# Optimization experiments

Measured on AMD Instinct MI355X. Metric: run time of the kernel, lower is better.

Reference implementation:

```python
import jax, jax.numpy as jnp
import numpy as np

B, NP, FEAT, DEG, H = 16, 1024, 512, 16, 1024
E = B * NP * DEG
RATIO = 0.8


def setup_inputs() -> dict:
    key = jax.random.key(0)
    ks = jax.random.split(key, 16)
    x = jax.random.normal(ks[0], (B * NP, FEAT), jnp.float32)
    g = jnp.repeat(jnp.arange(B, dtype=jnp.int32), NP * DEG)
    src = jax.random.randint(ks[1], (E,), 0, NP, jnp.int32) + g * NP
    dst = jax.random.randint(ks[2], (E,), 0, NP, jnp.int32) + g * NP
    edge_index = jnp.stack([src, dst])
    batch = jnp.repeat(jnp.arange(B, dtype=jnp.int32), NP)
    sc = 0.02
    inp = dict(x=x, edge_index=edge_index, batch=batch)
    # SAGEConv params: out = lin_l(mean_agg) + lin_r(x); bias only on lin_l (PyG default)
    inp['W1l'] = sc * jax.random.normal(ks[3], (H, FEAT), jnp.float32)
    inp['b1'] = jnp.zeros((H,), jnp.float32)
    inp['W1r'] = sc * jax.random.normal(ks[4], (H, FEAT), jnp.float32)
    inp['p1'] = jax.random.normal(ks[5], (H,), jnp.float32)
    inp['W2l'] = sc * jax.random.normal(ks[6], (H, H), jnp.float32)
    inp['b2'] = jnp.zeros((H,), jnp.float32)
    inp['W2r'] = sc * jax.random.normal(ks[7], (H, H), jnp.float32)
    inp['p2'] = jax.random.normal(ks[8], (H,), jnp.float32)
    inp['W3l'] = sc * jax.random.normal(ks[9], (H, H), jnp.float32)
    inp['b3'] = jnp.zeros((H,), jnp.float32)
    inp['W3r'] = sc * jax.random.normal(ks[10], (H, H), jnp.float32)
    inp['p3'] = jax.random.normal(ks[11], (H,), jnp.float32)
    return inp


def _sage(x, src, dst, w, Wl, b, Wr, n_nodes):
    # mean aggregation over (masked) incoming edges, isolated nodes -> 0
    deg = jax.ops.segment_sum(w, dst, num_segments=n_nodes)
    agg = jax.ops.segment_sum(x[src] * w[:, None], dst, num_segments=n_nodes)
    mean = agg / jnp.maximum(deg, 1.0)[:, None]
    return mean @ Wl.T + b + x @ Wr.T


def _topk_pool(x, src, dst, mask, p, n_per):
    # PyG TopKPooling: score = tanh((x.w)/||w||); keep top ceil(ratio*n) per graph
    k = int(np.ceil(RATIO * n_per))
    s = jnp.tanh((x @ p) / jnp.linalg.norm(p))
    vals, idx = jax.lax.top_k(s.reshape(B, n_per), k)          # [B,k]
    old = (idx + (jnp.arange(B, dtype=idx.dtype) * n_per)[:, None]).reshape(-1)
    x_new = x[old] * vals.reshape(-1)[:, None]                  # gate kept nodes by score
    remap = jnp.full((B * n_per,), -1, jnp.int32).at[old].set(jnp.arange(B * k, dtype=jnp.int32))
    s2, d2 = remap[src], remap[dst]
    m2 = mask & (s2 >= 0) & (d2 >= 0)                           # drop edges losing an endpoint
    return x_new, jnp.where(m2, s2, 0), jnp.where(m2, d2, 0), m2, k


def _readout(x, n_per):
    xr = x.reshape(B, n_per, H)
    return jnp.concatenate([xr.max(axis=1), xr.mean(axis=1)], axis=1)  # [B, 2H]


def reference(x, edge_index, batch, W1l, b1, W1r, p1, W2l, b2, W2r, p2, W3l, b3, W3r, p3):
    src, dst = edge_index[0], edge_index[1]
    mask = jnp.ones((src.shape[0],), bool)
    n = NP
    h = jax.nn.relu(_sage(x, src, dst, mask.astype(x.dtype), W1l, b1, W1r, B * n))
    h, src, dst, mask, n = _topk_pool(h, src, dst, mask, p1, n)
    x1 = _readout(h, n)
    h = jax.nn.relu(_sage(h, src, dst, mask.astype(h.dtype), W2l, b2, W2r, B * n))
    h, src, dst, mask, n = _topk_pool(h, src, dst, mask, p2, n)
    x2 = _readout(h, n)
    h = jax.nn.relu(_sage(h, src, dst, mask.astype(h.dtype), W3l, b3, W3r, B * n))
    h, src, dst, mask, n = _topk_pool(h, src, dst, mask, p3, n)
    x3 = _readout(h, n)
    return x1 + x2 + x3
```

## Files before the change

### kernel.cpp

```cpp
#include <hip/hip_runtime.h>
#include <math.h>

#define B_    16
#define NP_   1024
#define FEAT_ 512
#define H_    1024
#define E_    262144
#define EPG_  16384
#define K1_   820
#define K2_   656
#define K3_   525
#define M1_   16384
#define M2_   13120
#define M3_   10496
#define MP1_  16384
#define MP2_  13312
#define MP3_  11264
#define SPROWS_ 16384

typedef unsigned short ushort_t;
typedef __bf16 bf16x8 __attribute__((ext_vector_type(8)));
typedef float f32x4 __attribute__((ext_vector_type(4)));

__device__ inline ushort_t f2bf(float f) {
    unsigned u = __float_as_uint(f);
    u += 0x7FFF + ((u >> 16) & 1);
    return (ushort_t)(u >> 16);
}
__device__ inline float bf2f(ushort_t h) {
    return __uint_as_float(((unsigned)h) << 16);
}
__device__ inline void split1(float v, ushort_t& hi, ushort_t& lo) {
    hi = f2bf(v);
    lo = f2bf(v - bf2f(hi));
}

__device__ inline void gll16(const void* g, void* l) {
    __builtin_amdgcn_global_load_lds((__attribute__((address_space(1))) void*)g,
                                     (__attribute__((address_space(3))) void*)l, 16, 0, 0);
}


__global__ __launch_bounds__(1024) void prep2_kernel(const int* __restrict__ ei,
                                                     int* __restrict__ counts,
                                                     int* __restrict__ offsets,
                                                     int* __restrict__ adj,
                                                     const float* __restrict__ p1,
                                                     const float* __restrict__ p2,
                                                     const float* __restrict__ p3,
                                                     float* __restrict__ pnout,
                                                     const float* __restrict__ W1l, const float* __restrict__ W1r,
                                                     const float* __restrict__ W2l, const float* __restrict__ W2r,
                                                     const float* __restrict__ W3l, const float* __restrict__ W3r,
                                                     ushort_t* __restrict__ Wb1, ushort_t* __restrict__ Wb2,
                                                     ushort_t* __restrict__ Wb3) {
    int t = threadIdx.x;
    if (blockIdx.x < 16) {
        __shared__ int cnt[1024];
        __shared__ int scanb[1024];
        int b = blockIdx.x;
        int e0 = b * EPG_;
        cnt[t] = 0;
        __syncthreads();
        for (int e = e0 + t; e < e0 + EPG_; e += 1024)
            atomicAdd(&cnt[ei[E_ + e] - b * NP_], 1);
        __syncthreads();
        int v = cnt[t];
        scanb[t] = v;
        __syncthreads();
        for (int off = 1; off < 1024; off <<= 1) {
            int tv = (t >= off) ? scanb[t - off] : 0;
            __syncthreads();
            scanb[t] += tv;
            __syncthreads();
        }
        int excl = scanb[t] - v;
        counts[b * NP_ + t] = v;
        offsets[b * NP_ + t] = e0 + excl;
        cnt[t] = excl;
        __syncthreads();
        for (int e = e0 + t; e < e0 + EPG_; e += 1024) {
            int s = ei[e];
            int dloc = ei[E_ + e] - b * NP_;
            int pos = atomicAdd(&cnt[dloc], 1);
            adj[e0 + pos] = s;
        }
        return;
    }
    if (blockIdx.x < 19) {
        const float* p = blockIdx.x == 16 ? p1 : (blockIdx.x == 17 ? p2 : p3);
        __shared__ float red[1024];
        float a = p[t];
        red[t] = a * a;
        __syncthreads();
        for (int s = 512; s > 0; s >>= 1) {
            if (t < s) red[t] += red[t + s];
            __syncthreads();
        }
        if (t == 0) pnout[blockIdx.x - 16] = sqrtf(red[0]);
        return;
    }
    int idx = (blockIdx.x - 19) * 1024 + t;
    if (idx >= 524288 + 1048576 + 1048576) return;
    const float *Wl, *Wr; ushort_t* Wbig; int K;
    if (idx < 524288) { Wl = W1l; Wr = W1r; Wbig = Wb1; K = 512; }
    else if (idx < 524288 + 1048576) { idx -= 524288; Wl = W2l; Wr = W2r; Wbig = Wb2; K = 1024; }
    else { idx -= 524288 + 1048576; Wl = W3l; Wr = W3r; Wbig = Wb3; K = 1024; }
    int n = idx / K;
    int k = idx - n * K;
    ushort_t* row = Wbig + (size_t)n * (4 * K);
    float a = Wl[idx];
    ushort_t ah = f2bf(a);
    row[k] = ah;
    row[K + k] = f2bf(a - bf2f(ah));
    float b = Wr[idx];
    ushort_t bh = f2bf(b);
    row[2 * K + k] = bh;
    row[3 * K + k] = f2bf(b - bf2f(bh));
}


__global__ __launch_bounds__(128) void agg1_k512(const float* __restrict__ x,
                                                 const int* __restrict__ adj,
                                                 const int* __restrict__ offsets,
                                                 const int* __restrict__ counts,
                                                 ushort_t* __restrict__ Abig) {
    int gid = blockIdx.x;
    int xcd = gid & 7;
    int u = gid >> 3;
    int half = u & 1;
    int pi = u >> 1;
    int gsel = (pi >= 512) ? 1 : 0;
    int g = xcd + (gsel << 3);
    int node = g * 1024 + (pi - (gsel << 9)) * 2 + (threadIdx.x >> 6);
    int c = threadIdx.x & 63;
    int col4 = half * 64 + c;
    int start = offsets[node], cnt = counts[node];
    float d = fmaxf((float)cnt, 1.0f);
    const float4* xb = (const float4*)x;
    float ax = 0.f, ay = 0.f, az = 0.f, aw = 0.f;
    int j = 0;
    for (; j + 8 <= cnt; j += 8) {
        int si[8];
#pragma unroll
        for (int q = 0; q < 8; ++q) si[q] = adj[start + j + q];
        float4 vv[8];
#pragma unroll
        for (int q = 0; q < 8; ++q) vv[q] = xb[(size_t)si[q] * 128 + col4];
#pragma unroll
        for (int q = 0; q < 8; ++q) {
            ax += vv[q].x; ay += vv[q].y; az += vv[q].z; aw += vv[q].w;
        }
    }
    for (; j + 4 <= cnt; j += 4) {
        int s0 = adj[start + j + 0], s1 = adj[start + j + 1];
        int s2 = adj[start + j + 2], s3 = adj[start + j + 3];
        float4 v0 = xb[(size_t)s0 * 128 + col4];
        float4 v1 = xb[(size_t)s1 * 128 + col4];
        float4 v2 = xb[(size_t)s2 * 128 + col4];
        float4 v3 = xb[(size_t)s3 * 128 + col4];
        ax += (v0.x + v1.x) + (v2.x + v3.x);
        ay += (v0.y + v1.y) + (v2.y + v3.y);
        az += (v0.z + v1.z) + (v2.z + v3.z);
        aw += (v0.w + v1.w) + (v2.w + v3.w);
    }
    for (; j < cnt; ++j) {
        float4 v = xb[(size_t)adj[start + j] * 128 + col4];
        ax += v.x; ay += v.y; az += v.z; aw += v.w;
    }
    float inv = 1.0f / d;
    float4 cv = xb[(size_t)node * 128 + col4];
    ushort_t* row = Abig + (size_t)node * 2048;
    int f = col4 * 4;
    ushort4 mh, ml, ch, cl;
    split1(ax * inv, mh.x, ml.x); split1(ay * inv, mh.y, ml.y);
    split1(az * inv, mh.z, ml.z); split1(aw * inv, mh.w, ml.w);
    split1(cv.x, ch.x, cl.x); split1(cv.y, ch.y, cl.y);
    split1(cv.z, ch.z, cl.z); split1(cv.w, ch.w, cl.w);
    *(ushort4*)&row[f]        = mh;
    *(ushort4*)&row[512 + f]  = ml;
    *(ushort4*)&row[1024 + f] = ch;
    *(ushort4*)&row[1536 + f] = cl;
}

template<int LAYER>
__global__ __launch_bounds__(128) void agg23_k1024(const float* __restrict__ h,
                                                   const int* __restrict__ adj,
                                                   const int* __restrict__ offsets,
                                                   const int* __restrict__ counts,
                                                   const int* __restrict__ old_idx,
                                                   const float* __restrict__ vals,
                                                   ushort_t* __restrict__ Abig,
                                                   int n_per, int M, int npad) {
    int gid = blockIdx.x;
    if (gid >= 32 * n_per) {
        int r = gid - 32 * n_per;
        if (r < npad) {
            uint4* row = (uint4*)(Abig + (size_t)(M + r) * 4096);
#pragma unroll
            for (int q = 0; q < 4; ++q) row[threadIdx.x + q * 128] = (uint4){0, 0, 0, 0};
        }
        return;
    }
    int xcd = gid & 7;
    int u = gid >> 3;
    int half = u & 1;
    int nl = u >> 1;
    int gsel = (nl >= n_per) ? 1 : 0;
    int g = xcd + (gsel << 3);
    int node = g * n_per + nl - gsel * n_per;
    int c = threadIdx.x;
    int col4 = half * 128 + c;
    int start = offsets[node], cnt = counts[node];
    float d = fmaxf((float)cnt, 1.0f);
    const float4* hb = (const float4*)h;
    float ax = 0.f, ay = 0.f, az = 0.f, aw = 0.f;
    int j = 0;
    for (; j + 8 <= cnt; j += 8) {
        int si[8];
#pragma unroll
        for (int q = 0; q < 8; ++q) si[q] = adj[start + j + q];
        int oi[8]; float wi[8];
#pragma unroll
        for (int q = 0; q < 8; ++q) { oi[q] = old_idx[si[q]]; wi[q] = vals[si[q]]; }
        float4 vv[8];
#pragma unroll
        for (int q = 0; q < 8; ++q) vv[q] = hb[(size_t)oi[q] * 256 + col4];
#pragma unroll
        for (int q = 0; q < 8; ++q) {
            ax += wi[q] * vv[q].x; ay += wi[q] * vv[q].y;
            az += wi[q] * vv[q].z; aw += wi[q] * vv[q].w;
        }
    }
    for (; j + 4 <= cnt; j += 4) {
        int s0 = adj[start + j + 0], s1 = adj[start + j + 1];
        int s2 = adj[start + j + 2], s3 = adj[start + j + 3];
        int o0 = old_idx[s0], o1 = old_idx[s1], o2 = old_idx[s2], o3 = old_idx[s3];
        float w0 = vals[s0], w1 = vals[s1], w2 = vals[s2], w3 = vals[s3];
        float4 v0 = hb[(size_t)o0 * 256 + col4];
        float4 v1 = hb[(size_t)o1 * 256 + col4];
        float4 v2 = hb[(size_t)o2 * 256 + col4];
        float4 v3 = hb[(size_t)o3 * 256 + col4];
        ax += (w0 * v0.x + w1 * v1.x) + (w2 * v2.x + w3 * v3.x);
        ay += (w0 * v0.y + w1 * v1.y) + (w2 * v2.y + w3 * v3.y);
        az += (w0 * v0.z + w1 * v1.z) + (w2 * v2.z + w3 * v3.z);
        aw += (w0 * v0.w + w1 * v1.w) + (w2 * v2.w + w3 * v3.w);
    }
    for (; j < cnt; ++j) {
        int s = adj[start + j];
        int o = old_idx[s];
        float w = vals[s];
        float4 v = hb[(size_t)o * 256 + col4];
        ax += w * v.x; ay += w * v.y; az += w * v.z; aw += w * v.w;
    }
    float inv = 1.0f / d;
    int on = old_idx[node];
    float vn = vals[node];
    float4 cv = hb[(size_t)on * 256 + col4];
    cv.x *= vn; cv.y *= vn; cv.z *= vn; cv.w *= vn;
    ushort_t* row = Abig + (size_t)node * 4096;
    int f = col4 * 4;
    ushort4 mh, ml, ch, cl;
    split1(ax * inv, mh.x, ml.x); split1(ay * inv, mh.y, ml.y);
    split1(az * inv, mh.z, ml.z); split1(aw * inv, mh.w, ml.w);
    split1(cv.x, ch.x, cl.x); split1(cv.y, ch.y, cl.y);
    split1(cv.z, ch.z, cl.z); split1(cv.w, ch.w, cl.w);
    *(ushort4*)&row[f]        = mh;
    *(ushort4*)&row[1024 + f] = ml;
    *(ushort4*)&row[2048 + f] = ch;
    *(ushort4*)&row[3072 + f] = cl;
}


#define STR_(x) #x
#define VMW2_(n) asm volatile("s_waitcnt vmcnt(" STR_(n) ")" ::: "memory")
#define VMW(n) VMW2_(n)
#define BARM() do { __builtin_amdgcn_s_barrier(); asm volatile("" ::: "memory"); } while (0)

#define STG(Lw_, pl_, src_, c_) {                                                   \
    const ushort_t* s_ = (src_) + (c_);                                             \
    gll16(s_, (Lw_) + (pl_) * 8192);                                                \
    gll16(s_ + rstep, (Lw_) + (pl_) * 8192 + 4096);                                 \
}

#define MFQ(I0, Aarr, A0, Barr)                                                     \
    _Pragma("unroll")                                                               \
    for (int ii = 0; ii < 4; ++ii) {                                                \
        _Pragma("unroll")                                                           \
        for (int jj = 0; jj < 4; ++jj)                                              \
            acc[(I0) + ii][jj] = __builtin_amdgcn_mfma_f32_16x16x32_bf16(           \
                Aarr[(A0) + ii], Barr[jj], acc[(I0) + ii][jj], 0, 0, 0);            \
    }

#define CHUNK(t_, b_, stg_, vb_, v1_, v3_) do {                                     \
    int cn_ = ((t_) + 1 < NC2) ? ((t_) + 1) * 32 : 2 * KK + ((t_) + 1 - NC2) * 32;  \
    const ushort_t* Lr = L + (b_) * 32768;                                          \
    ushort_t* Lw = L + (1 - (b_)) * 32768 + tid * 8;                                \
    VMW(vb_);                                                                       \
    BARM();                                                                         \
    bf16x8 ah[8], al[8], bh[4], bl[4];                                              \
    _Pragma("unroll") for (int q = 0; q < 4; ++q)                                   \
        ah[q] = *(const bf16x8*)&Lr[aoff + q * 512];                                \
    _Pragma("unroll") for (int q = 0; q < 4; ++q)                                   \
        bh[q] = *(const bf16x8*)&Lr[16384 + boff + q * 512];                        \
                           \
    _Pragma("unroll") for (int q = 0; q < 4; ++q)                                   \
        ah[4 + q] = *(const bf16x8*)&Lr[aoff + (4 + q) * 512];                      \
    if (stg_) { STG(Lw, 0, Ag, cn_); }                                              \
    BARM();                                                                         \
    __builtin_amdgcn_s_setprio(1);                                                  \
    MFQ(0, ah, 0, bh);                                                              \
    __builtin_amdgcn_s_setprio(0);                                                  \
    VMW(v1_);                                                                       \
    BARM();                                                                         \
                           \
    _Pragma("unroll") for (int q = 0; q < 4; ++q)                                   \
        al[q] = *(const bf16x8*)&Lr[8192 + aoff + q * 512];                         \
    if (stg_) { STG(Lw, 2, Bg, cn_); }                                              \
    BARM();                                                                         \
    __builtin_amdgcn_s_setprio(1);                                                  \
    MFQ(4, ah, 4, bh);                                                              \
    __builtin_amdgcn_s_setprio(0);                                                  \
    BARM();                                                                         \
                           \
    _Pragma("unroll") for (int q = 0; q < 4; ++q)                                   \
        al[4 + q] = *(const bf16x8*)&Lr[8192 + aoff + (4 + q) * 512];               \
    if (stg_) { STG(Lw, 1, Ag + KK, cn_); }                                         \
    BARM();                                                                         \
    __builtin_amdgcn_s_setprio(1);                                                  \
    MFQ(0, al, 0, bh);                                                              \
    __builtin_amdgcn_s_setprio(0);                                                  \
    VMW(v3_);                                                                       \
    BARM();                                                                         \
                           \
    _Pragma("unroll") for (int q = 0; q < 4; ++q)                                   \
        bl[q] = *(const bf16x8*)&Lr[24576 + boff + q * 512];                        \
    if (stg_) { STG(Lw, 3, Bg + KK, cn_); }                                         \
    BARM();                                                                         \
    __builtin_amdgcn_s_setprio(1);                                                  \
    MFQ(4, al, 4, bh);                                                              \
    __builtin_amdgcn_s_setprio(0);                                                  \
    BARM();                                                                         \
                                   \
    __builtin_amdgcn_s_setprio(1);                                                  \
    MFQ(0, ah, 0, bl);                                                              \
    MFQ(4, ah, 4, bl);                                                              \
    __builtin_amdgcn_s_setprio(0);                                                  \
} while (0)

template<int KK>
__global__ __launch_bounds__(512, 2) void gemm256(const ushort_t* __restrict__ Ab,
                                                  const ushort_t* __restrict__ Wb,
                                                  const float* __restrict__ bias,
                                                  float* __restrict__ C,
                                                  float* __restrict__ sp,
                                                  const float* __restrict__ pvec,
                                                  int npanels) {
    constexpr int LD  = 4 * KK;
    constexpr int NC  = KK / 16;
    constexpr int NC2 = KK / 32;
    __shared__ ushort_t L[65536];

    int tid = threadIdx.x;
    int lane = tid & 63;
    int w = tid >> 6;
    int wm = w >> 2, wn = w & 3;

    int nb = npanels * 4;
    int per = nb >> 3;
    int bp = (blockIdx.x & 7) * per + (blockIdx.x >> 3);
    int panel = bp >> 2, cb = bp & 3;
    int m0 = panel * 256, n0 = cb * 256;

    int srow = tid >> 2;
    int gq = (tid & 3) ^ (srow & 3) ^ ((srow >> 2) & 3);
    const ushort_t* Ag = Ab + (size_t)(m0 + srow) * LD + gq * 8;
    const ushort_t* Bg = Wb + (size_t)(n0 + srow) * LD + gq * 8;
    const size_t rstep = (size_t)128 * LD;

    int qsw = (lane >> 4) ^ (lane & 3) ^ ((lane >> 2) & 3);
    int aoff = (wm * 128 + (lane & 15)) * 32 + qsw * 8;
    int boff = (wn * 64 + (lane & 15)) * 32 + qsw * 8;

    f32x4 acc[8][4];
#pragma unroll
    for (int i = 0; i < 8; ++i)
#pragma unroll
        for (int j = 0; j < 4; ++j) acc[i][j] = (f32x4){0.f, 0.f, 0.f, 0.f};

    {
        ushort_t* Lw0 = L + tid * 8;
        STG(Lw0, 0, Ag, 0);
        STG(Lw0, 2, Bg, 0);
        STG(Lw0, 1, Ag + KK, 0);
        STG(Lw0, 3, Bg + KK, 0);
    }

#pragma unroll 1
    for (int t = 0; t < NC - 2; t += 2) {
        CHUNK(t,     0, 1, 4, 4, 6);
        CHUNK(t + 1, 1, 1, 4, 4, 6);
    }
    CHUNK(NC - 2, 0, 1, 4, 4, 6);
    CHUNK(NC - 1, 1, 0, 4, 2, 0);

    float bj[4], pj[4];
#pragma unroll
    for (int j = 0; j < 4; ++j) {
        int col = n0 + wn * 64 + j * 16 + (lane & 15);
        bj[j] = bias[col];
        pj[j] = pvec[col];
    }
    int slot = cb * 4 + wn;
#pragma unroll
    for (int i = 0; i < 8; ++i) {
        int row0 = m0 + wm * 128 + i * 16 + (lane >> 4) * 4;
        float sacc[4] = {0.f, 0.f, 0.f, 0.f};
#pragma unroll
        for (int j = 0; j < 4; ++j) {
            int col = n0 + wn * 64 + j * 16 + (lane & 15);
#pragma unroll
            for (int r = 0; r < 4; ++r) {
                float v = acc[i][j][r] + bj[j];
                v = v > 0.f ? v : 0.f;
                C[(size_t)(row0 + r) * 1024 + col] = v;
                sacc[r] += v * pj[j];
            }
        }
#pragma unroll
        for (int r = 0; r < 4; ++r) {
            float sv_ = sacc[r];
            sv_ += __shfl_xor(sv_, 1);
            sv_ += __shfl_xor(sv_, 2);
            sv_ += __shfl_xor(sv_, 4);
            sv_ += __shfl_xor(sv_, 8);
            if ((lane & 15) == 0) sp[slot * SPROWS_ + row0 + r] = sv_;
        }
    }
}


template<int FIRST>
__global__ __launch_bounds__(1024) void tail_kernel(const float* __restrict__ sp,
                                                    const float* __restrict__ pn,
                                                    const float* __restrict__ h,
                                                    float* __restrict__ out,
                                                    int n, int k,
                                                    int* __restrict__ old_idx, float* __restrict__ vals,
                                                    const int* __restrict__ ei,
                                                    int* __restrict__ esrc, int* __restrict__ edst,
                                                    int* __restrict__ emask,
                                                    int* __restrict__ counts, int* __restrict__ offsets,
                                                    int* __restrict__ adj, int do_edges) {
    __shared__ float sv[1024];
    __shared__ int   rmap[1024];
    __shared__ int   oi_s[1024];
    __shared__ float vv_s[1024];
    __shared__ float4 rmx[32][32];
    __shared__ float4 rsm[32][32];
    int b = blockIdx.x / 9, role = blockIdx.x % 9;
    int t = threadIdx.x;
    if (role == 8 && !do_edges) return;

    float mine = -INFINITY;
    if (t < n) {
        int base = b * n + t;
        float s0 = 0.f;
#pragma unroll
        for (int c = 0; c < 16; ++c) s0 += sp[c * SPROWS_ + base];
        mine = s0;
    }
    sv[t] = mine;
    __syncthreads();
    int rank = 0;
#pragma unroll 4
    for (int j = 0; j < 1024; ++j) {
        float o = sv[j];
        rank += (o > mine) || (o == mine && j < t);
    }
    bool kept = (t < n) && (rank < k);
    rmap[t] = kept ? rank : -1;
    if (kept) {
        float tv = tanhf(mine / pn[0]);
        oi_s[rank] = b * n + t;
        vv_s[rank] = tv;
        if (role == 8) {
            old_idx[b * k + rank] = b * n + t;
            vals[b * k + rank] = tv;
        }
    }
    __syncthreads();

    if (role < 8) {
        int c32 = t & 31, g = t >> 5;
        int col4 = role * 32 + c32;
        const float4* hb = (const float4*)h;
        float4 mx = {-INFINITY, -INFINITY, -INFINITY, -INFINITY};
        float4 sm = {0.f, 0.f, 0.f, 0.f};
        for (int i = g; i < k; i += 32) {
            int o = oi_s[i];
            float wgt = vv_s[i];
            float4 v = hb[(size_t)o * 256 + col4];
            v.x *= wgt; v.y *= wgt; v.z *= wgt; v.w *= wgt;
            mx.x = fmaxf(mx.x, v.x); mx.y = fmaxf(mx.y, v.y);
            mx.z = fmaxf(mx.z, v.z); mx.w = fmaxf(mx.w, v.w);
            sm.x += v.x; sm.y += v.y; sm.z += v.z; sm.w += v.w;
        }
        rmx[g][c32] = mx; rsm[g][c32] = sm;
        __syncthreads();
        for (int s = 16; s > 0; s >>= 1) {
            if (g < s) {
                float4 om = rmx[g + s][c32], os = rsm[g + s][c32];
                float4 m = rmx[g][c32], ss2 = rsm[g][c32];
                m.x = fmaxf(m.x, om.x); m.y = fmaxf(m.y, om.y);
                m.z = fmaxf(m.z, om.z); m.w = fmaxf(m.w, om.w);
                ss2.x += os.x; ss2.y += os.y; ss2.z += os.z; ss2.w += os.w;
                rmx[g][c32] = m; rsm[g][c32] = ss2;
            }
            __syncthreads();
        }
        if (g == 0) {
            float4 m = rmx[0][c32], ss2 = rsm[0][c32];
            float invk = 1.0f / (float)k;
            float* o0 = out + (size_t)b * 2048 + col4 * 4;
            float* o1 = o0 + 1024;
            if (FIRST) {
                o0[0] = m.x; o0[1] = m.y; o0[2] = m.z; o0[3] = m.w;
                o1[0] = ss2.x * invk; o1[1] = ss2.y * invk;
                o1[2] = ss2.z * invk; o1[3] = ss2.w * invk;
            } else {
                o0[0] += m.x; o0[1] += m.y; o0[2] += m.z; o0[3] += m.w;
                o1[0] += ss2.x * invk; o1[1] += ss2.y * invk;
                o1[2] += ss2.z * invk; o1[3] += ss2.w * invk;
            }
        }
        return;
    }

    __shared__ int cnt_s[1024];
    cnt_s[t] = 0;
    __syncthreads();
    int e0 = b * EPG_;
    for (int e = e0 + t; e < e0 + EPG_; e += 1024) {
        int ms = FIRST ? 1 : emask[e];
        if (ms) {
            int s = FIRST ? ei[e] : esrc[e];
            int dd = FIRST ? ei[E_ + e] : edst[e];
            int ns = rmap[s - b * n];
            int nd = rmap[dd - b * n];
            if (ns >= 0 && nd >= 0) atomicAdd(&cnt_s[nd], 1);
        }
    }
    __syncthreads();
    int v = (t < k) ? cnt_s[t] : 0;
    oi_s[t] = v;
    __syncthreads();
    for (int off = 1; off < 1024; off <<= 1) {
        int tv = (t >= off) ? oi_s[t - off] : 0;
        __syncthreads();
        oi_s[t] += tv;
        __syncthreads();
    }
    int excl = oi_s[t] - v;
    if (t < k) {
        counts[b * k + t] = v;
        offsets[b * k + t] = e0 + excl;
        cnt_s[t] = excl;
    }
    __syncthreads();
    for (int e = e0 + t; e < e0 + EPG_; e += 1024) {
        int ms = FIRST ? 1 : emask[e];
        if (ms) {
            int s = FIRST ? ei[e] : esrc[e];
            int dd = FIRST ? ei[E_ + e] : edst[e];
            int ns = rmap[s - b * n];
            int nd = rmap[dd - b * n];
            if (ns >= 0 && nd >= 0) {
                int gs = b * k + ns;
                esrc[e] = gs;
                edst[e] = b * k + nd;
                if (FIRST) emask[e] = 1;
                int pos = atomicAdd(&cnt_s[nd], 1);
                adj[e0 + pos] = gs;
            } else {
                emask[e] = 0;
            }
        } else if (FIRST) {
            emask[e] = 0;
        }
    }
}


extern "C" void kernel_launch(void* const* d_in, const int* in_sizes, int n_in,
                              void* d_out, int out_size, void* d_ws, size_t ws_size,
                              hipStream_t stream) {
    const float* x   = (const float*)d_in[0];
    const int*   ei  = (const int*)d_in[1];
    const float* W1l = (const float*)d_in[3];
    const float* b1  = (const float*)d_in[4];
    const float* W1r = (const float*)d_in[5];
    const float* p1  = (const float*)d_in[6];
    const float* W2l = (const float*)d_in[7];
    const float* b2  = (const float*)d_in[8];
    const float* W2r = (const float*)d_in[9];
    const float* p2  = (const float*)d_in[10];
    const float* W3l = (const float*)d_in[11];
    const float* b3  = (const float*)d_in[12];
    const float* W3r = (const float*)d_in[13];
    const float* p3  = (const float*)d_in[14];
    float* out = (float*)d_out;

    char* ws = (char*)d_ws;
    size_t off = 0;
    float* bufOut = (float*)(ws + off); off += (size_t)MP1_ * 1024 * 4;
    ushort_t* Abig = (ushort_t*)(ws + off); off += (size_t)MP2_ * 4096 * 2;
    ushort_t* Wb1 = (ushort_t*)(ws + off); off += (size_t)1024 * 2048 * 2;
    ushort_t* Wb2 = (ushort_t*)(ws + off); off += (size_t)1024 * 4096 * 2;
    ushort_t* Wb3 = (ushort_t*)(ws + off); off += (size_t)1024 * 4096 * 2;
    float* sp = (float*)(ws + off); off += (size_t)16 * SPROWS_ * 4;
    char* misc = ws + off;
    int*   counts = (int*)(misc + 0 * 65536);
    int*   offsets= (int*)(misc + 1 * 65536);
    int*   old_idx= (int*)(misc + 2 * 65536);
    float* vals   = (float*)(misc + 3 * 65536);
    float* pnormv = (float*)(misc + 4 * 65536);
    int*   adj    = (int*)(misc + 5 * 65536);
    int*   esrc   = (int*)(misc + 5 * 65536 + 1 * 1048576);
    int*   edst   = (int*)(misc + 5 * 65536 + 2 * 1048576);
    int*   emask  = (int*)(misc + 5 * 65536 + 3 * 1048576);

    prep2_kernel<<<19 + (524288 + 2 * 1048576) / 1024, 1024, 0, stream>>>(
        ei, counts, offsets, adj, p1, p2, p3, pnormv,
        W1l, W1r, W2l, W2r, W3l, W3r, Wb1, Wb2, Wb3);

    agg1_k512<<<16384, 128, 0, stream>>>(x, adj, offsets, counts, Abig);
    gemm256<512><<<(MP1_ / 256) * 4, 512, 0, stream>>>(Abig, Wb1, b1, bufOut, sp, p1, MP1_ / 256);
    tail_kernel<1><<<B_ * 9, 1024, 0, stream>>>(sp, pnormv + 0, bufOut, out, NP_, K1_,
                                                old_idx, vals, ei, esrc, edst, emask,
                                                counts, offsets, adj, 1);

    agg23_k1024<2><<<32 * K1_ + (MP2_ - M2_), 128, 0, stream>>>(
        bufOut, adj, offsets, counts, old_idx, vals, Abig, K1_, M2_, MP2_ - M2_);
    gemm256<1024><<<(MP2_ / 256) * 4, 512, 0, stream>>>(Abig, Wb2, b2, bufOut, sp, p2, MP2_ / 256);
    tail_kernel<0><<<B_ * 9, 1024, 0, stream>>>(sp, pnormv + 1, bufOut, out, K1_, K2_,
                                                old_idx, vals, ei, esrc, edst, emask,
                                                counts, offsets, adj, 1);

    agg23_k1024<3><<<32 * K2_ + (MP3_ - M3_), 128, 0, stream>>>(
        bufOut, adj, offsets, counts, old_idx, vals, Abig, K2_, M3_, MP3_ - M3_);
    gemm256<1024><<<(MP3_ / 256) * 4, 512, 0, stream>>>(Abig, Wb3, b3, bufOut, sp, p3, MP3_ / 256);
    tail_kernel<0><<<B_ * 9, 1024, 0, stream>>>(sp, pnormv + 2, bufOut, out, K2_, K3_,
                                                old_idx, vals, ei, esrc, edst, emask,
                                                counts, offsets, adj, 0);
}
```

Baseline: 773.4 us.

## Load GEMM B operand directly from global into registers, halve LDS staging

Measured after the change: 934.0 us. +20.8%, slower.

```diff
diff --git a/kernel.cpp b/kernel.cpp
--- a/kernel.cpp
+++ b/kernel.cpp
@@ -292,57 +292,34 @@
                 Aarr[(A0) + ii], Barr[jj], acc[(I0) + ii][jj], 0, 0, 0);            \
     }
 
-#define CHUNK(t_, b_, stg_, vb_, v1_, v3_) do {                                     \
-    int cn_ = ((t_) + 1 < NC2) ? ((t_) + 1) * 32 : 2 * KK + ((t_) + 1 - NC2) * 32;  \
-    const ushort_t* Lr = L + (b_) * 32768;                                          \
-    ushort_t* Lw = L + (1 - (b_)) * 32768 + tid * 8;                                \
-    VMW(vb_);                                                                       \
+#define CHUNK(t_, b_, stg_) do {                                                    \
+    int cn_ = ((t_) < NC2) ? (t_) * 32 : 2 * KK + ((t_) - NC2) * 32;                \
+    int cs_ = ((t_) + 1 < NC2) ? ((t_) + 1) * 32 : 2 * KK + ((t_) + 1 - NC2) * 32;  \
+    const ushort_t* Lr = L + (b_) * 16384;                                          \
+    ushort_t* Lw = L + (1 - (b_)) * 16384 + tid * 8;                                \
+    VMW(2);                                                                         \
     BARM();                                                                         \
     bf16x8 ah[8], al[8], bh[4], bl[4];                                              \
-    _Pragma("unroll") for (int q = 0; q < 4; ++q)                                   \
+    _Pragma("unroll") for (int j = 0; j < 4; ++j)                                   \
+        bh[j] = *(const bf16x8*)(Bp[j] + cn_);                                      \
+    _Pragma("unroll") for (int q = 0; q < 8; ++q)                                   \
         ah[q] = *(const bf16x8*)&Lr[aoff + q * 512];                                \
-    _Pragma("unroll") for (int q = 0; q < 4; ++q)                                   \
-        bh[q] = *(const bf16x8*)&Lr[16384 + boff + q * 512];                        \
-                           \
-    _Pragma("unroll") for (int q = 0; q < 4; ++q)                                   \
-        ah[4 + q] = *(const bf16x8*)&Lr[aoff + (4 + q) * 512];                      \
-    if (stg_) { STG(Lw, 0, Ag, cn_); }                                              \
+    if (stg_) { STG(Lw, 0, Ag, cs_); }                                              \
     BARM();                                                                         \
     __builtin_amdgcn_s_setprio(1);                                                  \
     MFQ(0, ah, 0, bh);                                                              \
-    __builtin_amdgcn_s_setprio(0);                                                  \
-    VMW(v1_);                                                                       \
-    BARM();                                                                         \
-                           \
-    _Pragma("unroll") for (int q = 0; q < 4; ++q)                                   \
-        al[q] = *(const bf16x8*)&Lr[8192 + aoff + q * 512];                         \
-    if (stg_) { STG(Lw, 2, Bg, cn_); }                                              \
-    BARM();                                                                         \
-    __builtin_amdgcn_s_setprio(1);                                                  \
     MFQ(4, ah, 4, bh);                                                              \
     __builtin_amdgcn_s_setprio(0);                                                  \
     BARM();                                                                         \
-                           \
-    _Pragma("unroll") for (int q = 0; q < 4; ++q)                                   \
-        al[4 + q] = *(const bf16x8*)&Lr[8192 + aoff + (4 + q) * 512];               \
-    if (stg_) { STG(Lw, 1, Ag + KK, cn_); }                                         \
+    _Pragma("unroll") for (int j = 0; j < 4; ++j)                                   \
+        bl[j] = *(const bf16x8*)(Bp[j] + cn_ + KK);                                 \
+    _Pragma("unroll") for (int q = 0; q < 8; ++q)                                   \
+        al[q] = *(const bf16x8*)&Lr[8192 + aoff + q * 512];                         \
+    if (stg_) { STG(Lw, 1, Ag + KK, cs_); }                                         \
     BARM();                                                                         \
     __builtin_amdgcn_s_setprio(1);                                                  \
     MFQ(0, al, 0, bh);                                                              \
-    __builtin_amdgcn_s_setprio(0);                                                  \
-    VMW(v3_);                                                                       \
-    BARM();                                                                         \
-                           \
-    _Pragma("unroll") for (int q = 0; q < 4; ++q)                                   \
-        bl[q] = *(const bf16x8*)&Lr[24576 + boff + q * 512];                        \
-    if (stg_) { STG(Lw, 3, Bg + KK, cn_); }                                         \
-    BARM();                                                                         \
-    __builtin_amdgcn_s_setprio(1);                                                  \
     MFQ(4, al, 4, bh);                                                              \
-    __builtin_amdgcn_s_setprio(0);                                                  \
-    BARM();                                                                         \
-                                   \
-    __builtin_amdgcn_s_setprio(1);                                                  \
     MFQ(0, ah, 0, bl);                                                              \
     MFQ(4, ah, 4, bl);                                                              \
     __builtin_amdgcn_s_setprio(0);                                                  \
@@ -359,7 +336,7 @@
     constexpr int LD  = 4 * KK;
     constexpr int NC  = KK / 16;
     constexpr int NC2 = KK / 32;
-    __shared__ ushort_t L[65536];
+    __shared__ ushort_t L[32768];
 
     int tid = threadIdx.x;
     int lane = tid & 63;
@@ -375,12 +352,15 @@
     int srow = tid >> 2;
     int gq = (tid & 3) ^ (srow & 3) ^ ((srow >> 2) & 3);
     const ushort_t* Ag = Ab + (size_t)(m0 + srow) * LD + gq * 8;
-    const ushort_t* Bg = Wb + (size_t)(n0 + srow) * LD + gq * 8;
     const size_t rstep = (size_t)128 * LD;
 
     int qsw = (lane >> 4) ^ (lane & 3) ^ ((lane >> 2) & 3);
     int aoff = (wm * 128 + (lane & 15)) * 32 + qsw * 8;
-    int boff = (wn * 64 + (lane & 15)) * 32 + qsw * 8;
+
+    const ushort_t* Bp[4];
+#pragma unroll
+    for (int j = 0; j < 4; ++j)
+        Bp[j] = Wb + (size_t)(n0 + wn * 64 + j * 16 + (lane & 15)) * LD + (lane >> 4) * 8;
 
     f32x4 acc[8][4];
 #pragma unroll
@@ -391,18 +371,16 @@
     {
         ushort_t* Lw0 = L + tid * 8;
         STG(Lw0, 0, Ag, 0);
-        STG(Lw0, 2, Bg, 0);
         STG(Lw0, 1, Ag + KK, 0);
-        STG(Lw0, 3, Bg + KK, 0);
     }
 
 #pragma unroll 1
     for (int t = 0; t < NC - 2; t += 2) {
-        CHUNK(t,     0, 1, 4, 4, 6);
-        CHUNK(t + 1, 1, 1, 4, 4, 6);
-    }
-    CHUNK(NC - 2, 0, 1, 4, 4, 6);
-    CHUNK(NC - 1, 1, 0, 4, 2, 0);
+        CHUNK(t,     0, 1);
+        CHUNK(t + 1, 1, 1);
+    }
+    CHUNK(NC - 2, 0, 1);
+    CHUNK(NC - 1, 1, 0);
 
     float bj[4], pj[4];
 #pragma unroll
```
